# Kernel tuning notes

Measured on AMD Instinct MI355X. Metric: run time of the kernel, lower is better.

Reference implementation:

```python
import jax, jax.numpy as jnp
import numpy as np

DIM = 256
WS = 7
NUM_HEADS = 8
NW = 4096


def _relative_position_index(ws: int) -> jnp.ndarray:
    coords = jnp.stack(jnp.meshgrid(jnp.arange(ws), jnp.arange(ws), indexing='ij'))  # [2, ws, ws]
    flat = coords.reshape(2, -1)                                # [2, N]
    rel = flat[:, :, None] - flat[:, None, :]                   # [2, N, N]
    rel = rel.transpose(1, 2, 0) + (ws - 1)                     # [N, N, 2]
    rel = rel.at[:, :, 0].multiply(2 * ws - 1)
    return rel.sum(-1).astype(jnp.int32)                        # [N, N]


def setup_inputs() -> dict:
    key = jax.random.key(0)
    ks = jax.random.split(key, 7)
    N = WS * WS
    x_win = jax.random.normal(ks[0], (NW, N, DIM), dtype=jnp.float32)
    attn_mask = jnp.zeros((NW, N, N), dtype=jnp.float32)
    w_qkv = jax.random.normal(ks[1], (3 * DIM, DIM), dtype=jnp.float32) * (1.0 / np.sqrt(DIM))
    b_qkv = jax.random.normal(ks[2], (3 * DIM,), dtype=jnp.float32) * 0.02
    w_proj = jax.random.normal(ks[3], (DIM, DIM), dtype=jnp.float32) * (1.0 / np.sqrt(DIM))
    b_proj = jax.random.normal(ks[4], (DIM,), dtype=jnp.float32) * 0.02
    bias_table = jax.random.normal(ks[5], ((2 * WS - 1) * (2 * WS - 1), NUM_HEADS), dtype=jnp.float32)
    rel_index = _relative_position_index(WS)
    return {
        'x_win': x_win, 'attn_mask': attn_mask,
        'w_qkv': w_qkv, 'b_qkv': b_qkv,
        'w_proj': w_proj, 'b_proj': b_proj,
        'bias_table': bias_table, 'rel_index': rel_index,
    }


def reference(x_win, attn_mask, w_qkv, b_qkv, w_proj, b_proj, bias_table, rel_index):
    nW, N, C = x_win.shape
    H = bias_table.shape[-1]
    head_dim = C // H
    scale = 1.0 / np.sqrt(head_dim).astype(np.float32)

    # QKV projection (eqx.nn.Linear: y = W x + b)
    qkv = jnp.einsum('wnc,oc->wno', x_win, w_qkv) + b_qkv      # [nW, N, 3C]
    q, k, v = jnp.split(qkv, 3, axis=-1)

    def to_heads(t):
        return t.reshape(nW, N, H, head_dim).transpose(0, 2, 1, 3)  # [nW, H, N, d]

    q, k, v = to_heads(q), to_heads(k), to_heads(v)

    attn = jnp.einsum('whnd,whmd->whnm', q * scale, k)          # [nW, H, N, N]

    # Gathered relative position bias -> [H, N, N]
    bias = bias_table[rel_index.reshape(-1)].reshape(N, N, H).transpose(2, 0, 1)
    attn = attn + bias[None, :, :, :] + attn_mask[:, None, :, :]
    attn = jax.nn.softmax(attn, axis=-1)

    out = jnp.einsum('whnm,whmd->whnd', attn, v)                # [nW, H, N, d]
    out = out.transpose(0, 2, 1, 3).reshape(nW, N, C)
    out = jnp.einsum('wnc,oc->wno', out, w_proj) + b_proj
    return out
```

## Files before the change

### kernel.cpp

```cpp
#include <hip/hip_runtime.h>
#include <hip/hip_bf16.h>

typedef __bf16 bf16;
typedef bf16 bf16x4 __attribute__((ext_vector_type(4)));
typedef bf16 bf16x8 __attribute__((ext_vector_type(8)));
typedef float f32x4 __attribute__((ext_vector_type(4)));

#define MFMA16(a, b, c) __builtin_amdgcn_mfma_f32_16x16x32_bf16((a), (b), (c), 0, 0, 0)

constexpr int kN = 49, kC = 256;
constexpr float kScale = 0.17677669529663687f;

constexpr int WQKV_OFF = 0;
constexpr int WPROJ_OFF = 393216;
constexpr int BIAS_OFF = 524288;
constexpr int BQKV_OFF = 601120;

constexpr int XB_OFF = 0;
constexpr int QK_OFF = 25600;
constexpr int QS = 400;
constexpr int LDS_BYTES = 76800;

__global__ void prep_kernel(const float* __restrict__ w_qkv, const float* __restrict__ b_qkv,
                            const float* __restrict__ w_proj, const float* __restrict__ bias_table,
                            const int* __restrict__ rel_index, char* __restrict__ ws) {
  int i = blockIdx.x * 256 + threadIdx.x;
  bf16* wqkvb = (bf16*)(ws + WQKV_OFF);
  bf16* wprojb = (bf16*)(ws + WPROJ_OFF);
  float* biasx = (float*)(ws + BIAS_OFF);
  float* bqs = (float*)(ws + BQKV_OFF);
  if (i < 196608) {
    float v = w_qkv[i];
    if (i < 65536) v *= kScale;
    wqkvb[i] = (bf16)v;
  } else if (i < 262144) {
    int j = i - 196608;
    wprojb[j] = (bf16)w_proj[j];
  } else if (i < 281352) {
    int j = i - 262144;
    int h = j / 2401, nm = j - h * 2401;
    biasx[j] = bias_table[rel_index[nm] * 8 + h];
  } else if (i < 282120) {
    int j = i - 281352;
    bqs[j] = b_qkv[j] * (j < 256 ? kScale : 1.0f);
  }
}

__global__ __launch_bounds__(256, 2) void attn_kernel(
    const float* __restrict__ x, const float* __restrict__ mask, const float* __restrict__ b_proj,
    const char* __restrict__ ws, float* __restrict__ out) {
  extern __shared__ char smem[];
  bf16* xb = (bf16*)(smem + XB_OFF);
  bf16* qk = (bf16*)(smem + QK_OFF);

  const bf16* wqkvb = (const bf16*)(ws + WQKV_OFF);
  const bf16* wprojb = (const bf16*)(ws + WPROJ_OFF);
  const float* biasx = (const float*)(ws + BIAS_OFF);
  const float* bqs = (const float*)(ws + BQKV_OFF);

  const int tid = threadIdx.x;
  const int w = blockIdx.x;
  const int lane = tid & 63;
  const int wave = tid >> 6;
  const int g = lane >> 4;
  const int c = lane & 15;

  const float* xw = x + (size_t)w * (kN * kC);

#pragma unroll
  for (int it = 0; it < 13; ++it) {
    int idx = it * 256 + tid;
    if (idx < 3136) {
      int n = idx >> 6, c4 = (idx & 63) << 2;
      float4 v = ((const float4*)xw)[idx];
      bf16x4 b4;
      b4[0] = (bf16)v.x; b4[1] = (bf16)v.y; b4[2] = (bf16)v.z; b4[3] = (bf16)v.w;
      *(bf16x4*)(xb + ((c4 >> 3) * QS + n * 8 + (c4 & 7))) = b4;
    }
  }
  __syncthreads();

  for (int t = 0; t < 8; ++t) {
    int ot = wave * 8 + t;
    const bf16* ab = wqkvb + (ot * 16 + c) * 256 + g * 8;
    bf16x8 afr[8];
#pragma unroll
    for (int ks = 0; ks < 8; ++ks) afr[ks] = *(const bf16x8*)(ab + ks * 32);
    f32x4 acc[4] = {};
#pragma unroll
    for (int ks = 0; ks < 8; ++ks) {
      const bf16* bb = xb + (ks * 4 + g) * QS + c * 8;
#pragma unroll
      for (int nt = 0; nt < 4; ++nt) {
        bf16x8 bfr = *(const bf16x8*)(bb + nt * 128);
        acc[nt] = MFMA16(afr[ks], bfr, acc[nt]);
      }
    }
    int ob = ot * 16 + g * 4;
    float bq0 = bqs[ob], bq1 = bqs[ob + 1], bq2 = bqs[ob + 2], bq3 = bqs[ob + 3];
    int oc = ob >> 3, olow = ob & 7;
#pragma unroll
    for (int nt = 0; nt < 4; ++nt) {
      int n = nt * 16 + c;
      if (n < 50) {
        bool ok = (n < 49);
        bf16x4 pk;
        pk[0] = ok ? (bf16)(acc[nt][0] + bq0) : (bf16)0.f;
        pk[1] = ok ? (bf16)(acc[nt][1] + bq1) : (bf16)0.f;
        pk[2] = ok ? (bf16)(acc[nt][2] + bq2) : (bf16)0.f;
        pk[3] = ok ? (bf16)(acc[nt][3] + bq3) : (bf16)0.f;
        *(bf16x4*)(qk + (oc * QS + n * 8 + olow)) = pk;
      }
    }
  }

  bf16x8 va[2][2][2];
  for (int t = 0; t < 4; ++t) {
    int ct = wave * 4 + t;
    int o = 512 + ct * 16 + c;
    const bf16* bb = wqkvb + o * 256 + g * 8;
    bf16x8 bfr[8];
#pragma unroll
    for (int ks = 0; ks < 8; ++ks) bfr[ks] = *(const bf16x8*)(bb + ks * 32);
    f32x4 acc[4] = {};
#pragma unroll
    for (int ks = 0; ks < 8; ++ks) {
      const bf16* abL = xb + (ks * 4 + g) * QS + c * 8;
#pragma unroll
      for (int mt = 0; mt < 4; ++mt) {
        bf16x8 afr = *(const bf16x8*)(abL + mt * 128);
        acc[mt] = MFMA16(afr, bfr[ks], acc[mt]);
      }
    }
    float bv = bqs[o];
#pragma unroll
    for (int mt = 0; mt < 4; ++mt) {
      acc[mt][0] += bv; acc[mt][1] += bv; acc[mt][2] += bv; acc[mt][3] += bv;
    }
    int hh = t >> 1, dt = t & 1;
    int base = ((g & 1) * 2) * 16 + c;
#pragma unroll
    for (int ks = 0; ks < 2; ++ks) {
      f32x4 aL = acc[2 * ks], aH = acc[2 * ks + 1];
      float e[8];
#pragma unroll
      for (int i = 0; i < 4; ++i) {
        float xA = __shfl(aL[i], base), yA = __shfl(aH[i], base);
        float xB = __shfl(aL[i], base + 16), yB = __shfl(aH[i], base + 16);
        e[i] = (g < 2) ? xA : yA;
        e[4 + i] = (g < 2) ? xB : yB;
      }
      bf16x8 f;
#pragma unroll
      for (int j = 0; j < 8; ++j) {
        int m = ks * 32 + g * 8 + j;
        f[j] = (m < 49) ? (bf16)e[j] : (bf16)0.f;
      }
      va[hh][dt][ks] = f;
    }
  }
  __syncthreads();

  const int h0 = wave * 2;
  bf16x8 qa2[2][4], kb2[2][4];
#pragma unroll
  for (int hh = 0; hh < 2; ++hh) {
    int h = h0 + hh;
#pragma unroll
    for (int rt = 0; rt < 4; ++rt) {
      int n = rt * 16 + c; n = n > 49 ? 49 : n;
      qa2[hh][rt] = *(const bf16x8*)(qk + ((h * 4 + g) * QS + n * 8));
    }
#pragma unroll
    for (int mt = 0; mt < 4; ++mt) {
      int m = mt * 16 + c; m = m > 49 ? 49 : m;
      kb2[hh][mt] = *(const bf16x8*)(qk + ((32 + h * 4 + g) * QS + m * 8));
    }
  }
  __syncthreads();

  bf16* ptp = qk + wave * 4096;
  const float* mk = mask + (size_t)w * 2401;

  for (int hh = 0; hh < 2; ++hh) {
    int h = h0 + hh;
    const float* bh = biasx + h * 2401;
    f32x4 s[4][4] = {};
#pragma unroll
    for (int rt = 0; rt < 4; ++rt)
#pragma unroll
      for (int mt = 0; mt < 4; ++mt) s[rt][mt] = MFMA16(qa2[hh][rt], kb2[hh][mt], s[rt][mt]);

#pragma unroll
    for (int rt = 0; rt < 4; ++rt) {
      float pk_[4][4];
#pragma unroll
      for (int i = 0; i < 4; ++i) {
        int n = rt * 16 + g * 4 + i;
        bool nok = (n < 49);
        float vals[4];
#pragma unroll
        for (int mt = 0; mt < 4; ++mt) {
          int m = mt * 16 + c;
          float v = -1e30f;
          if (nok && m < 49) v = s[rt][mt][i] + bh[n * 49 + m] + mk[n * 49 + m];
          vals[mt] = v;
        }
        float mx = fmaxf(fmaxf(vals[0], vals[1]), fmaxf(vals[2], vals[3]));
        mx = fmaxf(mx, __shfl_xor(mx, 1));
        mx = fmaxf(mx, __shfl_xor(mx, 2));
        mx = fmaxf(mx, __shfl_xor(mx, 4));
        mx = fmaxf(mx, __shfl_xor(mx, 8));
        float p0 = __expf(vals[0] - mx), p1 = __expf(vals[1] - mx);
        float p2 = __expf(vals[2] - mx), p3 = __expf(vals[3] - mx);
        float sum = p0 + p1 + p2 + p3;
        sum += __shfl_xor(sum, 1);
        sum += __shfl_xor(sum, 2);
        sum += __shfl_xor(sum, 4);
        sum += __shfl_xor(sum, 8);
        float rinv = 1.0f / sum;
        pk_[0][i] = p0 * rinv; pk_[1][i] = p1 * rinv;
        pk_[2][i] = p2 * rinv; pk_[3][i] = p3 * rinv;
      }
#pragma unroll
      for (int mt = 0; mt < 4; ++mt) {
        int m = mt * 16 + c;
#pragma unroll
        for (int i = 0; i < 4; ++i) {
          int nl = g * 4 + i;
          ptp[rt * 1024 + nl * 64 + (m ^ (g << 4) ^ ((i & 1) << 3))] = (bf16)pk_[mt][i];
        }
      }
    }
    asm volatile("s_waitcnt lgkmcnt(0)" ::: "memory");

    f32x4 oacc[2][4] = {};
    const int xr = ((c >> 2) << 4) ^ ((c & 1) << 3);
#pragma unroll
    for (int nt = 0; nt < 4; ++nt) {
      const bf16* pr = ptp + nt * 1024 + c * 64;
      bf16x8 pb0 = *(const bf16x8*)(pr + ((g * 8) ^ xr));
      bf16x8 pb1 = *(const bf16x8*)(pr + ((32 + g * 8) ^ xr));
#pragma unroll
      for (int dt = 0; dt < 2; ++dt) {
        oacc[dt][nt] = MFMA16(va[hh][dt][0], pb0, oacc[dt][nt]);
        oacc[dt][nt] = MFMA16(va[hh][dt][1], pb1, oacc[dt][nt]);
      }
    }
#pragma unroll
    for (int dt = 0; dt < 2; ++dt) {
      int cb = h * 32 + dt * 16 + g * 4;
      int cc = cb >> 3, clow = cb & 7;
#pragma unroll
      for (int nt = 0; nt < 4; ++nt) {
        int n = nt * 16 + c;
        if (n < 49) {
          bf16x4 pk;
          pk[0] = (bf16)oacc[dt][nt][0]; pk[1] = (bf16)oacc[dt][nt][1];
          pk[2] = (bf16)oacc[dt][nt][2]; pk[3] = (bf16)oacc[dt][nt][3];
          *(bf16x4*)(xb + (cc * QS + n * 8 + clow)) = pk;
        }
      }
    }
  }
  __syncthreads();

  float* outw = out + (size_t)w * (kN * kC);
  for (int t = 0; t < 4; ++t) {
    int ct = wave * 4 + t;
    const bf16* bb = wprojb + (ct * 16 + c) * 256 + g * 8;
    bf16x8 bfr[8];
#pragma unroll
    for (int ks = 0; ks < 8; ++ks) bfr[ks] = *(const bf16x8*)(bb + ks * 32);
    f32x4 acc[4] = {};
#pragma unroll
    for (int ks = 0; ks < 8; ++ks) {
      const bf16* abL = xb + (ks * 4 + g) * QS + c * 8;
#pragma unroll
      for (int mt = 0; mt < 4; ++mt) {
        bf16x8 afr = *(const bf16x8*)(abL + mt * 128);
        acc[mt] = MFMA16(afr, bfr[ks], acc[mt]);
      }
    }
    float bp = b_proj[ct * 16 + c];
#pragma unroll
    for (int mt = 0; mt < 4; ++mt) {
#pragma unroll
      for (int i = 0; i < 4; ++i) {
        int n = mt * 16 + g * 4 + i;
        if (n < 49) outw[n * 256 + ct * 16 + c] = acc[mt][i] + bp;
      }
    }
  }
}

extern "C" void kernel_launch(void* const* d_in, const int* in_sizes, int n_in,
                              void* d_out, int out_size, void* d_ws, size_t ws_size,
                              hipStream_t stream) {
  const float* x = (const float*)d_in[0];
  const float* mask = (const float*)d_in[1];
  const float* w_qkv = (const float*)d_in[2];
  const float* b_qkv = (const float*)d_in[3];
  const float* w_proj = (const float*)d_in[4];
  const float* b_proj = (const float*)d_in[5];
  const float* bias_table = (const float*)d_in[6];
  const int* rel_index = (const int*)d_in[7];
  float* out = (float*)d_out;
  char* ws = (char*)d_ws;

  (void)in_sizes; (void)n_in; (void)out_size; (void)ws_size;

  hipFuncSetAttribute((const void*)attn_kernel, hipFuncAttributeMaxDynamicSharedMemorySize,
                      LDS_BYTES);

  prep_kernel<<<1103, 256, 0, stream>>>(w_qkv, b_qkv, w_proj, bias_table, rel_index, ws);
  attn_kernel<<<4096, 256, LDS_BYTES, stream>>>(x, mask, b_proj, ws, out);
}
```

Measured before the change: 510.7 us.

## Compute transposed scores to keep P in registers, stage output in LDS

Computes the score tile as K·Qᵀ so each softmax row lies within a column of lanes, uses cross-lane shuffles to build the P operand for the PV MFMA directly in registers, and drops the LDS round-trip for P along with its waitcnt. The bias table is precomputed in transposed order to fit the new access pattern. The projection output is written to a swizzled LDS buffer and then stored to global memory with coalesced float4 writes, replacing the strided scalar stores. This adds one extra barrier and more shuffle instructions, and the mask loads are now strided across lanes.

```diff
diff --git a/kernel.cpp b/kernel.cpp
--- a/kernel.cpp
+++ b/kernel.cpp
@@ -39,7 +39,8 @@
   } else if (i < 281352) {
     int j = i - 262144;
     int h = j / 2401, nm = j - h * 2401;
-    biasx[j] = bias_table[rel_index[nm] * 8 + h];
+    int mm = nm / 49, nn = nm - mm * 49;
+    biasx[j] = bias_table[rel_index[nn * 49 + mm] * 8 + h];
   } else if (i < 282120) {
     int j = i - 281352;
     bqs[j] = b_qkv[j] * (j < 256 ? kScale : 1.0f);
@@ -52,6 +53,7 @@
   extern __shared__ char smem[];
   bf16* xb = (bf16*)(smem + XB_OFF);
   bf16* qk = (bf16*)(smem + QK_OFF);
+  float* outf = (float*)(smem + QK_OFF);
 
   const bf16* wqkvb = (const bf16*)(ws + WQKV_OFF);
   const bf16* wprojb = (const bf16*)(ws + WPROJ_OFF);
@@ -162,91 +164,91 @@
   __syncthreads();
 
   const int h0 = wave * 2;
-  bf16x8 qa2[2][4], kb2[2][4];
+  const float* mk = mask + (size_t)w * 2401;
+
 #pragma unroll
   for (int hh = 0; hh < 2; ++hh) {
     int h = h0 + hh;
+    const float* bhT = biasx + h * 2401;
+
+    bf16x8 qa[4], kb[4];
 #pragma unroll
     for (int rt = 0; rt < 4; ++rt) {
       int n = rt * 16 + c; n = n > 49 ? 49 : n;
-      qa2[hh][rt] = *(const bf16x8*)(qk + ((h * 4 + g) * QS + n * 8));
+      qa[rt] = *(const bf16x8*)(qk + ((h * 4 + g) * QS + n * 8));
     }
 #pragma unroll
     for (int mt = 0; mt < 4; ++mt) {
       int m = mt * 16 + c; m = m > 49 ? 49 : m;
-      kb2[hh][mt] = *(const bf16x8*)(qk + ((32 + h * 4 + g) * QS + m * 8));
-    }
-  }
-  __syncthreads();
-
-  bf16* ptp = qk + wave * 4096;
-  const float* mk = mask + (size_t)w * 2401;
-
-  for (int hh = 0; hh < 2; ++hh) {
-    int h = h0 + hh;
-    const float* bh = biasx + h * 2401;
+      kb[mt] = *(const bf16x8*)(qk + ((32 + h * 4 + g) * QS + m * 8));
+    }
+
     f32x4 s[4][4] = {};
 #pragma unroll
-    for (int rt = 0; rt < 4; ++rt)
-#pragma unroll
-      for (int mt = 0; mt < 4; ++mt) s[rt][mt] = MFMA16(qa2[hh][rt], kb2[hh][mt], s[rt][mt]);
-
-#pragma unroll
-    for (int rt = 0; rt < 4; ++rt) {
-      float pk_[4][4];
-#pragma unroll
-      for (int i = 0; i < 4; ++i) {
-        int n = rt * 16 + g * 4 + i;
-        bool nok = (n < 49);
-        float vals[4];
-#pragma unroll
-        for (int mt = 0; mt < 4; ++mt) {
-          int m = mt * 16 + c;
-          float v = -1e30f;
-          if (nok && m < 49) v = s[rt][mt][i] + bh[n * 49 + m] + mk[n * 49 + m];
-          vals[mt] = v;
+    for (int mt = 0; mt < 4; ++mt)
+#pragma unroll
+      for (int nt = 0; nt < 4; ++nt) s[mt][nt] = MFMA16(kb[mt], qa[nt], s[mt][nt]);
+
+    f32x4 oacc[2][4] = {};
+#pragma unroll
+    for (int nt = 0; nt < 4; ++nt) {
+      int n = nt * 16 + c;
+      int nc = n > 48 ? 48 : n;
+      bool nok = (n < 49);
+      float vals[4][4];
+#pragma unroll
+      for (int mt = 0; mt < 4; ++mt)
+#pragma unroll
+        for (int i = 0; i < 4; ++i) {
+          int m = mt * 16 + g * 4 + i;
+          int mc2 = m > 48 ? 48 : m;
+          float bv = bhT[mc2 * 49 + nc];
+          float mv = mk[nc * 49 + mc2];
+          vals[mt][i] = (nok && m < 49) ? (s[mt][nt][i] + bv + mv) : -1e30f;
         }
-        float mx = fmaxf(fmaxf(vals[0], vals[1]), fmaxf(vals[2], vals[3]));
-        mx = fmaxf(mx, __shfl_xor(mx, 1));
-        mx = fmaxf(mx, __shfl_xor(mx, 2));
-        mx = fmaxf(mx, __shfl_xor(mx, 4));
-        mx = fmaxf(mx, __shfl_xor(mx, 8));
-        float p0 = __expf(vals[0] - mx), p1 = __expf(vals[1] - mx);
-        float p2 = __expf(vals[2] - mx), p3 = __expf(vals[3] - mx);
-        float sum = p0 + p1 + p2 + p3;
-        sum += __shfl_xor(sum, 1);
-        sum += __shfl_xor(sum, 2);
-        sum += __shfl_xor(sum, 4);
-        sum += __shfl_xor(sum, 8);
-        float rinv = 1.0f / sum;
-        pk_[0][i] = p0 * rinv; pk_[1][i] = p1 * rinv;
-        pk_[2][i] = p2 * rinv; pk_[3][i] = p3 * rinv;
-      }
-#pragma unroll
-      for (int mt = 0; mt < 4; ++mt) {
-        int m = mt * 16 + c;
+      float mx = vals[0][0];
+#pragma unroll
+      for (int mt = 0; mt < 4; ++mt)
+#pragma unroll
+        for (int i = 0; i < 4; ++i) mx = fmaxf(mx, vals[mt][i]);
+      mx = fmaxf(mx, __shfl_xor(mx, 16));
+      mx = fmaxf(mx, __shfl_xor(mx, 32));
+      float p_[4][4];
+      float sum = 0.f;
+#pragma unroll
+      for (int mt = 0; mt < 4; ++mt)
 #pragma unroll
         for (int i = 0; i < 4; ++i) {
-          int nl = g * 4 + i;
-          ptp[rt * 1024 + nl * 64 + (m ^ (g << 4) ^ ((i & 1) << 3))] = (bf16)pk_[mt][i];
+          float pv = __expf(vals[mt][i] - mx);
+          p_[mt][i] = pv;
+          sum += pv;
         }
-      }
-    }
-    asm volatile("s_waitcnt lgkmcnt(0)" ::: "memory");
-
-    f32x4 oacc[2][4] = {};
-    const int xr = ((c >> 2) << 4) ^ ((c & 1) << 3);
-#pragma unroll
-    for (int nt = 0; nt < 4; ++nt) {
-      const bf16* pr = ptp + nt * 1024 + c * 64;
-      bf16x8 pb0 = *(const bf16x8*)(pr + ((g * 8) ^ xr));
-      bf16x8 pb1 = *(const bf16x8*)(pr + ((32 + g * 8) ^ xr));
-#pragma unroll
-      for (int dt = 0; dt < 2; ++dt) {
-        oacc[dt][nt] = MFMA16(va[hh][dt][0], pb0, oacc[dt][nt]);
-        oacc[dt][nt] = MFMA16(va[hh][dt][1], pb1, oacc[dt][nt]);
-      }
-    }
+      sum += __shfl_xor(sum, 16);
+      sum += __shfl_xor(sum, 32);
+      float rinv = nok ? (1.0f / sum) : 0.0f;
+#pragma unroll
+      for (int mt = 0; mt < 4; ++mt)
+#pragma unroll
+        for (int i = 0; i < 4; ++i) p_[mt][i] *= rinv;
+
+#pragma unroll
+      for (int ks = 0; ks < 2; ++ks) {
+        float e[8];
+#pragma unroll
+        for (int j = 0; j < 8; ++j) {
+          int src = ((g & 1) * 2 + (j >> 2)) * 16 + c;
+          float vA = __shfl(p_[2 * ks][j & 3], src);
+          float vB = __shfl(p_[2 * ks + 1][j & 3], src);
+          e[j] = (g < 2) ? vA : vB;
+        }
+        bf16x8 f;
+#pragma unroll
+        for (int j = 0; j < 8; ++j) f[j] = (bf16)e[j];
+#pragma unroll
+        for (int dt = 0; dt < 2; ++dt) oacc[dt][nt] = MFMA16(va[hh][dt][ks], f, oacc[dt][nt]);
+      }
+    }
+
 #pragma unroll
     for (int dt = 0; dt < 2; ++dt) {
       int cb = h * 32 + dt * 16 + g * 4;
@@ -265,7 +267,6 @@
   }
   __syncthreads();
 
-  float* outw = out + (size_t)w * (kN * kC);
   for (int t = 0; t < 4; ++t) {
     int ct = wave * 4 + t;
     const bf16* bb = wprojb + (ct * 16 + c) * 256 + g * 8;
@@ -283,13 +284,26 @@
       }
     }
     float bp = b_proj[ct * 16 + c];
+    int co = ct * 16 + c, q = co >> 2, c3 = co & 3;
 #pragma unroll
     for (int mt = 0; mt < 4; ++mt) {
 #pragma unroll
       for (int i = 0; i < 4; ++i) {
         int n = mt * 16 + g * 4 + i;
-        if (n < 49) outw[n * 256 + ct * 16 + c] = acc[mt][i] + bp;
-      }
+        if (n < 49) outf[n * 256 + ((q ^ (n & 15)) << 2) + c3] = acc[mt][i] + bp;
+      }
+    }
+  }
+  __syncthreads();
+
+  float4* outw4 = (float4*)(out + (size_t)w * (kN * kC));
+  const float4* outf4 = (const float4*)outf;
+#pragma unroll
+  for (int it = 0; it < 13; ++it) {
+    int f = it * 256 + tid;
+    if (f < 3136) {
+      int n = f >> 6, q = f & 63;
+      outw4[f] = outf4[n * 64 + (q ^ (n & 15))];
     }
   }
 }
```

Result: faster. 431.0 us (-15.6%).
